# Performance work log

Hardware: AMD Instinct MI355X
Metric: run time of the kernel (lower is better)

Reference implementation:

```python
import jax, jax.numpy as jnp
import numpy as np
import math

D_MODEL = 1024
N_HEAD = 16
D_HEAD = D_MODEL // N_HEAD


def setup_inputs() -> dict:
    key = jax.random.key(0)
    k0, k1, k2, k3, k4 = jax.random.split(key, 5)
    B, N = 4, 2048
    inp = jax.random.normal(k0, (B, N, D_MODEL), dtype=jnp.float32)
    # causal mask: True = keep (masked_fill on ~mask)
    mask = jnp.tril(jnp.ones((N, N), dtype=bool))
    # qkv_proj Linear(d_model, 3*d_model); output Linear(d_model, d_model)
    s_in = 1.0 / math.sqrt(D_MODEL)
    W_qkv = jax.random.uniform(k1, (D_MODEL, 3 * D_MODEL), jnp.float32, -s_in, s_in)
    b_qkv = jax.random.uniform(k2, (3 * D_MODEL,), jnp.float32, -s_in, s_in)
    W_out = jax.random.uniform(k3, (D_MODEL, D_MODEL), jnp.float32, -s_in, s_in)
    b_out = jax.random.uniform(k4, (D_MODEL,), jnp.float32, -s_in, s_in)
    return {"input": inp, "W_qkv": W_qkv, "b_qkv": b_qkv,
            "W_out": W_out, "b_out": b_out, "mask": mask}


def reference(input, W_qkv, b_qkv, W_out, b_out, mask):
    B, N, d = input.shape
    qkv = input @ W_qkv + b_qkv                       # [B,N,3d]  (dropout=eval no-op)
    q, k, v = jnp.split(qkv, 3, axis=-1)
    # [B,N,H,Dh] -> [B,H,N,Dh]
    q = q.reshape(B, N, N_HEAD, D_HEAD).transpose(0, 2, 1, 3)
    k = k.reshape(B, N, N_HEAD, D_HEAD).transpose(0, 2, 1, 3)
    v = v.reshape(B, N, N_HEAD, D_HEAD).transpose(0, 2, 1, 3)
    scale = 1.0 / math.sqrt(D_HEAD)
    scores = jnp.einsum('bhqd,bhkd->bhqk', q, k) * scale   # [B,H,N,N]
    scores = jnp.where(mask, scores, -jnp.inf)
    attn = jax.nn.softmax(scores, axis=-1)
    out = jnp.einsum('bhqk,bhkd->bhqd', attn, v)           # [B,H,N,Dh]
    out = out.transpose(0, 2, 1, 3).reshape(B, N, d)       # concat heads
    return out @ W_out + b_out
```

## Files before the change

### kernel.cpp

```cpp
#include <hip/hip_runtime.h>
#include <hip/hip_bf16.h>

typedef unsigned short u16;
typedef unsigned u32;
typedef __attribute__((ext_vector_type(4))) unsigned short u16x4;
typedef __attribute__((ext_vector_type(8))) unsigned short u16x8;
typedef __attribute__((ext_vector_type(4))) unsigned u32x4;
typedef __attribute__((ext_vector_type(8))) __bf16 bf16x8;
typedef __attribute__((ext_vector_type(4))) float f32x4;

typedef __attribute__((address_space(1))) void as1v;
typedef __attribute__((address_space(3))) void as3v;

#define MFMA16(a, b, c) __builtin_amdgcn_mfma_f32_16x16x32_bf16(a, b, c, 0, 0, 0)

#if __has_builtin(__builtin_amdgcn_permlane16_swap) && __has_builtin(__builtin_amdgcn_permlane32_swap)
#define HAVE_PERMLANE_SWAP 1
#else
#define HAVE_PERMLANE_SWAP 0
#endif

__device__ __forceinline__ u16 f2bf(float f) {
    unsigned u = __builtin_bit_cast(unsigned, f);
    u += 0x7fffu + ((u >> 16) & 1u);
    return (u16)(u >> 16);
}

__device__ __forceinline__ u32 pkbf(float lo, float hi) {
    u32 r;
    asm("v_cvt_pk_bf16_f32 %0, %1, %2" : "=v"(r) : "v"(lo), "v"(hi));
    return r;
}

__device__ __forceinline__ void gload16(const void* g, void* l) {
    __builtin_amdgcn_global_load_lds((as1v*)g, (as3v*)l, 16, 0, 0);
}

__device__ __forceinline__ float redmax_cross(float v) {
#if HAVE_PERMLANE_SWAP
    u32 xu = __builtin_bit_cast(u32, v);
    auto r16 = __builtin_amdgcn_permlane16_swap(xu, xu, false, false);
    float a = fmaxf(__builtin_bit_cast(float, (u32)r16[0]),
                    __builtin_bit_cast(float, (u32)r16[1]));
    u32 au = __builtin_bit_cast(u32, a);
    auto r32 = __builtin_amdgcn_permlane32_swap(au, au, false, false);
    return fmaxf(__builtin_bit_cast(float, (u32)r32[0]),
                 __builtin_bit_cast(float, (u32)r32[1]));
#else
    v = fmaxf(v, __shfl_xor(v, 16, 64));
    return fmaxf(v, __shfl_xor(v, 32, 64));
#endif
}

__device__ __forceinline__ float redsum_cross(float v) {
#if HAVE_PERMLANE_SWAP
    u32 xu = __builtin_bit_cast(u32, v);
    auto r16 = __builtin_amdgcn_permlane16_swap(xu, xu, false, false);
    float a = __builtin_bit_cast(float, (u32)r16[0]) +
              __builtin_bit_cast(float, (u32)r16[1]);
    u32 au = __builtin_bit_cast(u32, a);
    auto r32 = __builtin_amdgcn_permlane32_swap(au, au, false, false);
    return __builtin_bit_cast(float, (u32)r32[0]) +
           __builtin_bit_cast(float, (u32)r32[1]);
#else
    v += __shfl_xor(v, 16, 64);
    return v + __shfl_xor(v, 32, 64);
#endif
}

__global__ void convert_f32_bf16(const float* __restrict__ in, u16* __restrict__ out, int n4) {
    int i = blockIdx.x * blockDim.x + threadIdx.x;
    if (i < n4) {
        float4 v = *(const float4*)&in[(size_t)i * 4];
        u16x4 o;
        o.x = f2bf(v.x); o.y = f2bf(v.y); o.z = f2bf(v.z); o.w = f2bf(v.w);
        *(u16x4*)&out[(size_t)i * 4] = o;
    }
}

__global__ void transpose_convert(const float* __restrict__ in, u16* __restrict__ out, int R, int C) {
    __shared__ float tl[64][65];
    const int rb = blockIdx.x, cb = blockIdx.y;
    const int tid = threadIdx.x;
    for (int it = 0; it < 4; ++it) {
        int lin = (tid + it * 256) * 4;
        int r = lin >> 6, c = lin & 63;
        float4 v = *(const float4*)&in[(size_t)(rb * 64 + r) * C + cb * 64 + c];
        tl[r][c + 0] = v.x; tl[r][c + 1] = v.y; tl[r][c + 2] = v.z; tl[r][c + 3] = v.w;
    }
    __syncthreads();
    for (int it = 0; it < 4; ++it) {
        int lin = (tid + it * 256) * 4;
        int oc = lin >> 6, orr = lin & 63;
        u16x4 o;
        o.x = f2bf(tl[orr + 0][oc]);
        o.y = f2bf(tl[orr + 1][oc]);
        o.z = f2bf(tl[orr + 2][oc]);
        o.w = f2bf(tl[orr + 3][oc]);
        *(u16x4*)&out[(size_t)(cb * 64 + oc) * R + rb * 64 + orr] = o;
    }
}

__global__ void transpose_v(const u16* __restrict__ vbuf, u16* __restrict__ vtb) {
    __shared__ u16 tl[64][65];
    const int nb = blockIdx.x, bh = blockIdx.y;
    const int tid = threadIdx.x;
    for (int it = 0; it < 2; ++it) {
        int lin = (tid + it * 256) * 8;
        int nl = lin >> 6, dh = lin & 63;
        u16x8 v = *(const u16x8*)&vbuf[((size_t)bh * 2048 + nb * 64 + nl) * 64 + dh];
#pragma unroll
        for (int j = 0; j < 8; ++j) tl[dh + j][nl] = v[j];
    }
    __syncthreads();
    for (int it = 0; it < 2; ++it) {
        int lin = (tid + it * 256) * 8;
        int dh = lin >> 6, nl = lin & 63;
        u16x8 o;
#pragma unroll
        for (int j = 0; j < 8; ++j) o[j] = tl[dh][nl + j];
        *(u16x8*)&vtb[((size_t)bh * 64 + dh) * 2048 + nb * 64 + nl] = o;
    }
}

__global__ __launch_bounds__(512, 2) void gemm256_qkv(
    const u16* __restrict__ A, const u16* __restrict__ Bt, const float* __restrict__ bias,
    u16* __restrict__ qb, u16* __restrict__ kb, u16* __restrict__ vb) {
    constexpr int K = 1024;
    constexpr int NT = 32;
    __shared__ u16 ldsu[49152];

    const int bid = blockIdx.x;
    const int swz = (bid & 7) * 96 + (bid >> 3);
    const int bm = swz / 24, bn = swz % 24;

    const int tid = threadIdx.x, wid = tid >> 6, lane = tid & 63;
    const int wr = wid >> 2, wc = wid & 3;
    const int l15 = lane & 15, lhi = lane >> 4;

    const int sslot = (lane & 7) ^ (lane >> 3);
    const int kcol = (sslot & 3) * 8;
    const int mloc = (lane >> 3) * 2 + (sslot >> 2);

    const u16* Arow[2];
#pragma unroll
    for (int li = 0; li < 2; ++li) {
        int sg = wid * 2 + li;
        Arow[li] = A + (size_t)(bm * 256 + sg * 16 + mloc) * K + kcol;
    }
    const u16* Brow = Bt + (size_t)(bn * 128 + wid * 16 + mloc) * K + kcol;

    auto stageA = [&](int buf, int t) {
#pragma unroll
        for (int li = 0; li < 2; ++li) {
            int sg = wid * 2 + li;
            gload16(Arow[li] + t * 32, (char*)ldsu + buf * 24576 + sg * 1024);
        }
    };
    auto stageB = [&](int buf, int t) {
        gload16(Brow + t * 32, (char*)ldsu + buf * 24576 + 16384 + wid * 1024);
    };

    const int rslot = ((l15 & 1) * 4 + lhi) ^ ((l15 >> 1) & 7);
    const int fragoff = (l15 >> 1) * 64 + rslot * 8;

    f32x4 acc[8][2];
#pragma unroll
    for (int i = 0; i < 8; ++i) {
        acc[i][0] = (f32x4){0.f, 0.f, 0.f, 0.f};
        acc[i][1] = (f32x4){0.f, 0.f, 0.f, 0.f};
    }

    auto doTile = [&](int cur, int tstage, bool dostage) {
        const u16* Ab = ldsu + cur * 12288 + wr * 4096 + fragoff;
        const u16* Bb = ldsu + cur * 12288 + 8192 + wc * 1024 + fragoff;
        bf16x8 af[8], b0, b1;
#pragma unroll
        for (int mf = 0; mf < 8; ++mf) af[mf] = *(const bf16x8*)(Ab + mf * 512);
        b0 = *(const bf16x8*)(Bb);
        b1 = *(const bf16x8*)(Bb + 512);
        if (dostage) stageA(tstage & 3, tstage);
        __builtin_amdgcn_s_setprio(1);
#pragma unroll
        for (int mf = 0; mf < 8; ++mf) acc[mf][0] = MFMA16(af[mf], b0, acc[mf][0]);
        __builtin_amdgcn_s_setprio(0);
        if (dostage) stageB(tstage & 3, tstage);
        __builtin_amdgcn_s_setprio(1);
#pragma unroll
        for (int mf = 0; mf < 8; ++mf) acc[mf][1] = MFMA16(af[mf], b1, acc[mf][1]);
        __builtin_amdgcn_s_setprio(0);
    };

    stageA(0, 0); stageB(0, 0);
    stageA(1, 1); stageB(1, 1);
    stageA(2, 2); stageB(2, 2);
    asm volatile("s_waitcnt vmcnt(6)" ::: "memory");
    __builtin_amdgcn_s_barrier();
    __builtin_amdgcn_sched_barrier(0);

    for (int t = 0; t < NT - 3; ++t) {
        doTile(t & 3, t + 3, true);
        asm volatile("s_waitcnt vmcnt(6)" ::: "memory");
        __builtin_amdgcn_s_barrier();
        __builtin_amdgcn_sched_barrier(0);
    }
    doTile((NT - 3) & 3, 0, false);
    asm volatile("s_waitcnt vmcnt(3)" ::: "memory");
    __builtin_amdgcn_s_barrier();
    __builtin_amdgcn_sched_barrier(0);
    doTile((NT - 2) & 3, 0, false);
    asm volatile("s_waitcnt vmcnt(0)" ::: "memory");
    __builtin_amdgcn_s_barrier();
    __builtin_amdgcn_sched_barrier(0);
    doTile((NT - 1) & 3, 0, false);

    __syncthreads();
    const int cg0 = bn * 128 + wc * 32;
    const int which = cg0 >> 10, rem = cg0 & 1023;
    u16* dst = (which == 0) ? qb : (which == 1) ? kb : vb;
    const float qs = (which == 0) ? 0.18033688011112042f : 1.0f;
    const int hh = rem >> 6, dh0 = rem & 63;
    const int rgb0 = bm * 256 + wr * 128;
    const int bb = rgb0 >> 11, n0 = rgb0 & 2047;
    char* lep = (char*)ldsu + wid * 8192;
    float bv0 = bias[cg0 + l15], bv1 = bias[cg0 + 16 + l15];
#pragma unroll
    for (int mf = 0; mf < 8; ++mf)
#pragma unroll
        for (int v = 0; v < 4; ++v) {
            int row = mf * 16 + lhi * 4 + v;
            int sw = ((row >> 2) & 3) << 4;
            *(u16*)(lep + row * 64 + ((l15 * 2) ^ sw)) =
                f2bf((acc[mf][0][v] + bv0) * qs);
            *(u16*)(lep + row * 64 + ((32 + l15 * 2) ^ sw)) =
                f2bf((acc[mf][1][v] + bv1) * qs);
        }
    const size_t gbase = (((size_t)bb * 16 + hh) * 2048 + n0) * 64 + dh0;
#pragma unroll
    for (int it = 0; it < 8; ++it) {
        int idx = it * 64 + lane;
        int row = idx >> 2, j = idx & 3;
        u16x8 vv = *(const u16x8*)(lep + row * 64 + ((j * 16) ^ (((row >> 2) & 3) << 4)));
        *(u16x8*)&dst[gbase + (size_t)row * 64 + j * 8] = vv;
    }
}

__global__ __launch_bounds__(512, 2) void gemm256_out(
    const u16* __restrict__ A, const u16* __restrict__ Bt, const float* __restrict__ bias,
    float* __restrict__ outf) {
    constexpr int K = 1024;
    constexpr int NT = 32;
    __shared__ u16 ldsu[49152];

    const int bid = blockIdx.x;
    const int swz = (bid & 7) * 32 + (bid >> 3);
    const int bm = swz >> 3, bn = swz & 7;

    const int tid = threadIdx.x, wid = tid >> 6, lane = tid & 63;
    const int wr = wid >> 2, wc = wid & 3;
    const int l15 = lane & 15, lhi = lane >> 4;

    const int sslot = (lane & 7) ^ (lane >> 3);
    const int kcol = (sslot & 3) * 8;
    const int mloc = (lane >> 3) * 2 + (sslot >> 2);

    const u16* Arow[2];
#pragma unroll
    for (int li = 0; li < 2; ++li) {
        int sg = wid * 2 + li;
        Arow[li] = A + (size_t)(bm * 256 + sg * 16 + mloc) * K + kcol;
    }
    const u16* Brow = Bt + (size_t)(bn * 128 + wid * 16 + mloc) * K + kcol;

    auto stageA = [&](int buf, int t) {
#pragma unroll
        for (int li = 0; li < 2; ++li) {
            int sg = wid * 2 + li;
            gload16(Arow[li] + t * 32, (char*)ldsu + buf * 24576 + sg * 1024);
        }
    };
    auto stageB = [&](int buf, int t) {
        gload16(Brow + t * 32, (char*)ldsu + buf * 24576 + 16384 + wid * 1024);
    };

    const int rslot = ((l15 & 1) * 4 + lhi) ^ ((l15 >> 1) & 7);
    const int fragoff = (l15 >> 1) * 64 + rslot * 8;

    f32x4 acc[8][2];
#pragma unroll
    for (int i = 0; i < 8; ++i) {
        acc[i][0] = (f32x4){0.f, 0.f, 0.f, 0.f};
        acc[i][1] = (f32x4){0.f, 0.f, 0.f, 0.f};
    }

    auto doTile = [&](int cur, int tstage, bool dostage) {
        const u16* Ab = ldsu + cur * 12288 + wr * 4096 + fragoff;
        const u16* Bb = ldsu + cur * 12288 + 8192 + wc * 1024 + fragoff;
        bf16x8 af[8], b0, b1;
#pragma unroll
        for (int mf = 0; mf < 8; ++mf) af[mf] = *(const bf16x8*)(Ab + mf * 512);
        b0 = *(const bf16x8*)(Bb);
        b1 = *(const bf16x8*)(Bb + 512);
        if (dostage) stageA(tstage & 3, tstage);
        __builtin_amdgcn_s_setprio(1);
#pragma unroll
        for (int mf = 0; mf < 8; ++mf) acc[mf][0] = MFMA16(af[mf], b0, acc[mf][0]);
        __builtin_amdgcn_s_setprio(0);
        if (dostage) stageB(tstage & 3, tstage);
        __builtin_amdgcn_s_setprio(1);
#pragma unroll
        for (int mf = 0; mf < 8; ++mf) acc[mf][1] = MFMA16(af[mf], b1, acc[mf][1]);
        __builtin_amdgcn_s_setprio(0);
    };

    stageA(0, 0); stageB(0, 0);
    stageA(1, 1); stageB(1, 1);
    stageA(2, 2); stageB(2, 2);
    asm volatile("s_waitcnt vmcnt(6)" ::: "memory");
    __builtin_amdgcn_s_barrier();
    __builtin_amdgcn_sched_barrier(0);

    for (int t = 0; t < NT - 3; ++t) {
        doTile(t & 3, t + 3, true);
        asm volatile("s_waitcnt vmcnt(6)" ::: "memory");
        __builtin_amdgcn_s_barrier();
        __builtin_amdgcn_sched_barrier(0);
    }
    doTile((NT - 3) & 3, 0, false);
    asm volatile("s_waitcnt vmcnt(3)" ::: "memory");
    __builtin_amdgcn_s_barrier();
    __builtin_amdgcn_sched_barrier(0);
    doTile((NT - 2) & 3, 0, false);
    asm volatile("s_waitcnt vmcnt(0)" ::: "memory");
    __builtin_amdgcn_s_barrier();
    __builtin_amdgcn_sched_barrier(0);
    doTile((NT - 1) & 3, 0, false);

#pragma unroll
    for (int nf = 0; nf < 2; ++nf) {
        int cg = bn * 128 + wc * 32 + nf * 16 + l15;
        float bv = bias[cg];
#pragma unroll
        for (int mf = 0; mf < 8; ++mf) {
            int rgb = bm * 256 + wr * 128 + mf * 16 + lhi * 4;
#pragma unroll
            for (int v = 0; v < 4; ++v)
                outf[(size_t)(rgb + v) * 1024 + cg] = acc[mf][nf][v] + bv;
        }
    }
}

__global__ __launch_bounds__(256, 4) void attn_kernel(
    const u16* __restrict__ qbuf, const u16* __restrict__ kbuf,
    const u16* __restrict__ vtb, u16* __restrict__ obuf) {
    __shared__ u16 Kl[2][64 * 64];
    __shared__ u16 Vl[2][64 * 64];
    const int bid = blockIdx.x;
    const int rr = bid >> 8;
    const int pp = (bid >> 6) & 3;
    const int c = (rr & 1) ? (((rr >> 1) << 2) + pp)
                           : (15 - ((rr >> 1) << 2) - pp);
    const int bh = ((bid & 7) << 3) + ((bid >> 3) & 7);
    const int b = bh >> 4, h = bh & 15;
    const int tid = threadIdx.x, wid = tid >> 6, lane = tid & 63;
    const int l15 = lane & 15, lhi = lane >> 4;
    const int q0 = c * 128 + wid * 32;
    const int ntW = 2 * c + (wid >> 1) + 1;
    const int ntmax = 2 * c + 2;

    auto loadQ = [&](int qbase, bf16x8* dst) {
        const u16* qp = qbuf + ((size_t)bh * 2048 + qbase + l15) * 64 + lhi * 8;
        dst[0] = *(const bf16x8*)(qp);
        dst[1] = *(const bf16x8*)(qp + 32);
    };
    bf16x8 qf0[2], qf1[2];
    loadQ(q0, qf0); loadQ(q0 + 16, qf1);

    float m0 = -1e30f, l0 = 0.f, m1 = -1e30f, l1 = 0.f;
    f32x4 o0[4], o1[4];
#pragma unroll
    for (int d = 0; d < 4; ++d) {
        o0[d] = (f32x4){0.f, 0.f, 0.f, 0.f};
        o1[d] = (f32x4){0.f, 0.f, 0.f, 0.f};
    }

    const int srow = lane >> 3;
    const int scolb = ((lane & 7) * 16) ^ (srow << 4);

    auto stage = [&](int buf, int t) {
        const int kbase = t * 64;
#pragma unroll
        for (int s = 0; s < 2; ++s) {
            int sg = wid * 2 + s;
            int row = sg * 8 + srow;
            const u16* gk = kbuf + ((size_t)bh * 2048 + kbase + row) * 64 + (scolb >> 1);
            gload16(gk, (char*)Kl[buf] + sg * 1024);
            const u16* gv = vtb + ((size_t)bh * 64 + row) * 2048 + kbase + (scolb >> 1);
            gload16(gv, (char*)Vl[buf] + sg * 1024);
        }
    };

    auto smax = [&](f32x4* s, int qg0, int t, float& m, float& l, f32x4* oa, u32* pw) {
        const int qg = qg0 + l15;
        if (64 * t + 63 > qg0) {
#pragma unroll
            for (int kb4 = 0; kb4 < 4; ++kb4)
#pragma unroll
                for (int v = 0; v < 4; ++v) {
                    int kg = 64 * t + kb4 * 16 + lhi * 4 + v;
                    if (kg > qg) s[kb4][v] = -1e30f;
                }
        }
        float pm = fmaxf(fmaxf(fmaxf(s[0][0], s[0][1]), fmaxf(s[0][2], s[0][3])),
                         fmaxf(fmaxf(s[1][0], s[1][1]), fmaxf(s[1][2], s[1][3])));
        pm = fmaxf(pm, fmaxf(fmaxf(fmaxf(s[2][0], s[2][1]), fmaxf(s[2][2], s[2][3])),
                             fmaxf(fmaxf(s[3][0], s[3][1]), fmaxf(s[3][2], s[3][3]))));
        pm = redmax_cross(pm);
        if (!__all(pm <= m + 8.f)) {
            float nm = fmaxf(m, pm);
            float f = exp2f(m - nm);
            m = nm;
            l *= f;
#pragma unroll
            for (int d = 0; d < 4; ++d)
#pragma unroll
                for (int v = 0; v < 4; ++v) oa[d][v] *= f;
        }
        float rs = 0.f;
#pragma unroll
        for (int kb4 = 0; kb4 < 4; ++kb4)
#pragma unroll
            for (int v = 0; v < 4; ++v) {
                float e = exp2f(s[kb4][v] - m);
                s[kb4][v] = e;
                rs += e;
            }
        l += redsum_cross(rs);
        pw[0] = pkbf(s[0][0], s[0][1]); pw[1] = pkbf(s[0][2], s[0][3]);
        pw[2] = pkbf(s[1][0], s[1][1]); pw[3] = pkbf(s[1][2], s[1][3]);
        pw[4] = pkbf(s[2][0], s[2][1]); pw[5] = pkbf(s[2][2], s[2][3]);
        pw[6] = pkbf(s[3][0], s[3][1]); pw[7] = pkbf(s[3][2], s[3][3]);
    };

    auto computeChunk = [&](const char* Kb, const char* Vb, int t) {
        f32x4 s0[4], s1[4];
        __builtin_amdgcn_s_setprio(1);
#pragma unroll
        for (int kb4 = 0; kb4 < 4; ++kb4) {
            const int r = kb4 * 16 + l15;
            const int sw = (r & 7) << 4;
            const int rowb = r * 128;
            bf16x8 kf0 = *(const bf16x8*)(Kb + rowb + ((lhi * 16) ^ sw));
            bf16x8 kf1 = *(const bf16x8*)(Kb + rowb + ((64 + lhi * 16) ^ sw));
            f32x4 a0 = (f32x4){0.f, 0.f, 0.f, 0.f};
            a0 = MFMA16(kf0, qf0[0], a0);
            a0 = MFMA16(kf1, qf0[1], a0);
            s0[kb4] = a0;
            f32x4 a1 = (f32x4){0.f, 0.f, 0.f, 0.f};
            a1 = MFMA16(kf0, qf1[0], a1);
            a1 = MFMA16(kf1, qf1[1], a1);
            s1[kb4] = a1;
        }
        __builtin_amdgcn_s_setprio(0);
        u32 pw0[8], pw1[8];
        smax(s0, q0, t, m0, l0, o0, pw0);
        smax(s1, q0 + 16, t, m1, l1, o1, pw1);
        __builtin_amdgcn_s_setprio(1);
#pragma unroll
        for (int ks = 0; ks < 2; ++ks) {
            bf16x8 pb0 = __builtin_bit_cast(bf16x8,
                (u32x4){pw0[ks * 4 + 0], pw0[ks * 4 + 1], pw0[ks * 4 + 2], pw0[ks * 4 + 3]});
            bf16x8 pb1 = __builtin_bit_cast(bf16x8,
                (u32x4){pw1[ks * 4 + 0], pw1[ks * 4 + 1], pw1[ks * 4 + 2], pw1[ks * 4 + 3]});
#pragma unroll
            for (int dhb = 0; dhb < 4; ++dhb) {
                const int r = dhb * 16 + l15;
                const int sw = (r & 7) << 4;
                u16x4 v0 = *(const u16x4*)(Vb + r * 128 + ((ks * 64 + 8 * lhi) ^ sw));
                u16x4 v1 = *(const u16x4*)(Vb + r * 128 + ((ks * 64 + 32 + 8 * lhi) ^ sw));
                u16x8 vv = {v0[0], v0[1], v0[2], v0[3], v1[0], v1[1], v1[2], v1[3]};
                bf16x8 vf = __builtin_bit_cast(bf16x8, vv);
                o0[dhb] = MFMA16(vf, pb0, o0[dhb]);
                o1[dhb] = MFMA16(vf, pb1, o1[dhb]);
            }
        }
        __builtin_amdgcn_s_setprio(0);
    };

    stage(0, 0);
    int t = 0;
    for (;;) {
        __syncthreads();
        if (t + 1 < ntmax) stage(1, t + 1);
        if (t < ntW) computeChunk((const char*)Kl[0], (const char*)Vl[0], t);
        if (++t == ntmax) break;
        __syncthreads();
        if (t + 1 < ntmax) stage(0, t + 1);
        if (t < ntW) computeChunk((const char*)Kl[1], (const char*)Vl[1], t);
        if (++t == ntmax) break;
    }

    auto epi = [&](int qg0, float l, const f32x4* oa) {
        const float rl = 1.f / l;
        const int q = qg0 + l15;
        const size_t rowoff = ((size_t)b * 2048 + q) * 1024 + h * 64;
#pragma unroll
        for (int dhb = 0; dhb < 4; ++dhb) {
            u16x4 w;
#pragma unroll
            for (int v = 0; v < 4; ++v) w[v] = f2bf(oa[dhb][v] * rl);
            *(u16x4*)&obuf[rowoff + dhb * 16 + lhi * 4] = w;
        }
    };
    epi(q0, l0, o0);
    epi(q0 + 16, l1, o1);
}

extern "C" void kernel_launch(void* const* d_in, const int* in_sizes, int n_in,
                              void* d_out, int out_size, void* d_ws, size_t ws_size,
                              hipStream_t stream) {
    const float* inp   = (const float*)d_in[0];
    const float* W_qkv = (const float*)d_in[1];
    const float* b_qkv = (const float*)d_in[2];
    const float* W_out = (const float*)d_in[3];
    const float* b_out = (const float*)d_in[4];
    float* out = (float*)d_out;

    u16* xb   = (u16*)d_ws;
    u16* wqt  = xb + 8388608;
    u16* wot  = wqt + 3145728;
    u16* qbuf = wot + 1048576;
    u16* kbuf = qbuf + 8388608;
    u16* vbuf = kbuf + 8388608;
    u16* vtb  = vbuf + 8388608;
    u16* obuf = vtb + 8388608;

    convert_f32_bf16<<<8192, 256, 0, stream>>>(inp, xb, 2097152);
    transpose_convert<<<dim3(16, 48), 256, 0, stream>>>(W_qkv, wqt, 1024, 3072);
    transpose_convert<<<dim3(16, 16), 256, 0, stream>>>(W_out, wot, 1024, 1024);
    gemm256_qkv<<<768, 512, 0, stream>>>(xb, wqt, b_qkv, qbuf, kbuf, vbuf);
    transpose_v<<<dim3(32, 64), 256, 0, stream>>>(vbuf, vtb);
    attn_kernel<<<1024, 256, 0, stream>>>(qbuf, kbuf, vtb, obuf);
    gemm256_out<<<256, 512, 0, stream>>>(obuf, wot, b_out, out);
}
```

Measured before the change: 186.5 us.

## Write V transposed from QKV GEMM epilogue and compute row sums via MFMA

```diff
diff --git a/kernel.cpp b/kernel.cpp
--- a/kernel.cpp
+++ b/kernel.cpp
@@ -101,31 +101,9 @@
     }
 }
 
-__global__ void transpose_v(const u16* __restrict__ vbuf, u16* __restrict__ vtb) {
-    __shared__ u16 tl[64][65];
-    const int nb = blockIdx.x, bh = blockIdx.y;
-    const int tid = threadIdx.x;
-    for (int it = 0; it < 2; ++it) {
-        int lin = (tid + it * 256) * 8;
-        int nl = lin >> 6, dh = lin & 63;
-        u16x8 v = *(const u16x8*)&vbuf[((size_t)bh * 2048 + nb * 64 + nl) * 64 + dh];
-#pragma unroll
-        for (int j = 0; j < 8; ++j) tl[dh + j][nl] = v[j];
-    }
-    __syncthreads();
-    for (int it = 0; it < 2; ++it) {
-        int lin = (tid + it * 256) * 8;
-        int dh = lin >> 6, nl = lin & 63;
-        u16x8 o;
-#pragma unroll
-        for (int j = 0; j < 8; ++j) o[j] = tl[dh][nl + j];
-        *(u16x8*)&vtb[((size_t)bh * 64 + dh) * 2048 + nb * 64 + nl] = o;
-    }
-}
-
 __global__ __launch_bounds__(512, 2) void gemm256_qkv(
     const u16* __restrict__ A, const u16* __restrict__ Bt, const float* __restrict__ bias,
-    u16* __restrict__ qb, u16* __restrict__ kb, u16* __restrict__ vb) {
+    u16* __restrict__ qb, u16* __restrict__ kb, u16* __restrict__ vtb) {
     constexpr int K = 1024;
     constexpr int NT = 32;
     __shared__ u16 ldsu[49152];
@@ -217,31 +195,48 @@
     __syncthreads();
     const int cg0 = bn * 128 + wc * 32;
     const int which = cg0 >> 10, rem = cg0 & 1023;
-    u16* dst = (which == 0) ? qb : (which == 1) ? kb : vb;
-    const float qs = (which == 0) ? 0.18033688011112042f : 1.0f;
     const int hh = rem >> 6, dh0 = rem & 63;
     const int rgb0 = bm * 256 + wr * 128;
     const int bb = rgb0 >> 11, n0 = rgb0 & 2047;
-    char* lep = (char*)ldsu + wid * 8192;
     float bv0 = bias[cg0 + l15], bv1 = bias[cg0 + 16 + l15];
-#pragma unroll
-    for (int mf = 0; mf < 8; ++mf)
-#pragma unroll
-        for (int v = 0; v < 4; ++v) {
-            int row = mf * 16 + lhi * 4 + v;
-            int sw = ((row >> 2) & 3) << 4;
-            *(u16*)(lep + row * 64 + ((l15 * 2) ^ sw)) =
-                f2bf((acc[mf][0][v] + bv0) * qs);
-            *(u16*)(lep + row * 64 + ((32 + l15 * 2) ^ sw)) =
-                f2bf((acc[mf][1][v] + bv1) * qs);
-        }
-    const size_t gbase = (((size_t)bb * 16 + hh) * 2048 + n0) * 64 + dh0;
-#pragma unroll
-    for (int it = 0; it < 8; ++it) {
-        int idx = it * 64 + lane;
-        int row = idx >> 2, j = idx & 3;
-        u16x8 vv = *(const u16x8*)(lep + row * 64 + ((j * 16) ^ (((row >> 2) & 3) << 4)));
-        *(u16x8*)&dst[gbase + (size_t)row * 64 + j * 8] = vv;
+
+    if (which == 2) {
+        const size_t vbase = ((size_t)(bb * 16 + hh) * 64 + dh0) * 2048 + (size_t)n0;
+#pragma unroll
+        for (int nf = 0; nf < 2; ++nf) {
+            float bv = (nf == 0) ? bv0 : bv1;
+            size_t rowb = vbase + (size_t)(nf * 16 + l15) * 2048;
+#pragma unroll
+            for (int mf = 0; mf < 8; ++mf) {
+                u16x4 w;
+#pragma unroll
+                for (int v = 0; v < 4; ++v) w[v] = f2bf(acc[mf][nf][v] + bv);
+                *(u16x4*)&vtb[rowb + mf * 16 + lhi * 4] = w;
+            }
+        }
+    } else {
+        u16* dst = (which == 0) ? qb : kb;
+        const float qs = (which == 0) ? 0.18033688011112042f : 1.0f;
+        char* lep = (char*)ldsu + wid * 8192;
+#pragma unroll
+        for (int mf = 0; mf < 8; ++mf)
+#pragma unroll
+            for (int v = 0; v < 4; ++v) {
+                int row = mf * 16 + lhi * 4 + v;
+                int sw = ((row >> 2) & 3) << 4;
+                *(u16*)(lep + row * 64 + ((l15 * 2) ^ sw)) =
+                    f2bf((acc[mf][0][v] + bv0) * qs);
+                *(u16*)(lep + row * 64 + ((32 + l15 * 2) ^ sw)) =
+                    f2bf((acc[mf][1][v] + bv1) * qs);
+            }
+        const size_t gbase = (((size_t)bb * 16 + hh) * 2048 + n0) * 64 + dh0;
+#pragma unroll
+        for (int it = 0; it < 8; ++it) {
+            int idx = it * 64 + lane;
+            int row = idx >> 2, j = idx & 3;
+            u16x8 vv = *(const u16x8*)(lep + row * 64 + ((j * 16) ^ (((row >> 2) & 3) << 4)));
+            *(u16x8*)&dst[gbase + (size_t)row * 64 + j * 8] = vv;
+        }
     }
 }
 
@@ -376,13 +371,24 @@
     bf16x8 qf0[2], qf1[2];
     loadQ(q0, qf0); loadQ(q0 + 16, qf1);
 
-    float m0 = -1e30f, l0 = 0.f, m1 = -1e30f, l1 = 0.f;
-    f32x4 o0[4], o1[4];
+    bf16x8 onesA;
+    {
+        u16x8 ov;
+        u16 o = (l15 == 0) ? (u16)0x3F80 : (u16)0;
+#pragma unroll
+        for (int j = 0; j < 8; ++j) ov[j] = o;
+        onesA = __builtin_bit_cast(bf16x8, ov);
+    }
+
+    float m0 = -1e30f, m1 = -1e30f;
+    f32x4 o0[4], o1[4], lac0, lac1;
 #pragma unroll
     for (int d = 0; d < 4; ++d) {
         o0[d] = (f32x4){0.f, 0.f, 0.f, 0.f};
         o1[d] = (f32x4){0.f, 0.f, 0.f, 0.f};
     }
+    lac0 = (f32x4){0.f, 0.f, 0.f, 0.f};
+    lac1 = (f32x4){0.f, 0.f, 0.f, 0.f};
 
     const int srow = lane >> 3;
     const int scolb = ((lane & 7) * 16) ^ (srow << 4);
@@ -400,7 +406,7 @@
         }
     };
 
-    auto smax = [&](f32x4* s, int qg0, int t, float& m, float& l, f32x4* oa, u32* pw) {
+    auto smax = [&](f32x4* s, int qg0, int t, float& m, f32x4& lac, f32x4* oa, u32* pw) {
         const int qg = qg0 + l15;
         if (64 * t + 63 > qg0) {
 #pragma unroll
@@ -411,31 +417,29 @@
                     if (kg > qg) s[kb4][v] = -1e30f;
                 }
         }
-        float pm = fmaxf(fmaxf(fmaxf(s[0][0], s[0][1]), fmaxf(s[0][2], s[0][3])),
-                         fmaxf(fmaxf(s[1][0], s[1][1]), fmaxf(s[1][2], s[1][3])));
-        pm = fmaxf(pm, fmaxf(fmaxf(fmaxf(s[2][0], s[2][1]), fmaxf(s[2][2], s[2][3])),
-                             fmaxf(fmaxf(s[3][0], s[3][1]), fmaxf(s[3][2], s[3][3]))));
-        pm = redmax_cross(pm);
+        float f1 = fmaxf(fmaxf(s[0][0], s[0][1]), s[0][2]);
+        float f2 = fmaxf(fmaxf(s[0][3], s[1][0]), s[1][1]);
+        float f3 = fmaxf(fmaxf(s[1][2], s[1][3]), s[2][0]);
+        float f4 = fmaxf(fmaxf(s[2][1], s[2][2]), s[2][3]);
+        float f5 = fmaxf(fmaxf(s[3][0], s[3][1]), s[3][2]);
+        float g1 = fmaxf(fmaxf(f1, f2), f3);
+        float g2 = fmaxf(fmaxf(f4, f5), s[3][3]);
+        float pm = redmax_cross(fmaxf(g1, g2));
         if (!__all(pm <= m + 8.f)) {
             float nm = fmaxf(m, pm);
             float f = exp2f(m - nm);
             m = nm;
-            l *= f;
+#pragma unroll
+            for (int v = 0; v < 4; ++v) lac[v] *= f;
 #pragma unroll
             for (int d = 0; d < 4; ++d)
 #pragma unroll
                 for (int v = 0; v < 4; ++v) oa[d][v] *= f;
         }
-        float rs = 0.f;
 #pragma unroll
         for (int kb4 = 0; kb4 < 4; ++kb4)
 #pragma unroll
-            for (int v = 0; v < 4; ++v) {
-                float e = exp2f(s[kb4][v] - m);
-                s[kb4][v] = e;
-                rs += e;
-            }
-        l += redsum_cross(rs);
+            for (int v = 0; v < 4; ++v) s[kb4][v] = exp2f(s[kb4][v] - m);
         pw[0] = pkbf(s[0][0], s[0][1]); pw[1] = pkbf(s[0][2], s[0][3]);
         pw[2] = pkbf(s[1][0], s[1][1]); pw[3] = pkbf(s[1][2], s[1][3]);
         pw[4] = pkbf(s[2][0], s[2][1]); pw[5] = pkbf(s[2][2], s[2][3]);
@@ -463,8 +467,8 @@
         }
         __builtin_amdgcn_s_setprio(0);
         u32 pw0[8], pw1[8];
-        smax(s0, q0, t, m0, l0, o0, pw0);
-        smax(s1, q0 + 16, t, m1, l1, o1, pw1);
+        smax(s0, q0, t, m0, lac0, o0, pw0);
+        smax(s1, q0 + 16, t, m1, lac1, o1, pw1);
         __builtin_amdgcn_s_setprio(1);
 #pragma unroll
         for (int ks = 0; ks < 2; ++ks) {
@@ -483,6 +487,8 @@
                 o0[dhb] = MFMA16(vf, pb0, o0[dhb]);
                 o1[dhb] = MFMA16(vf, pb1, o1[dhb]);
             }
+            lac0 = MFMA16(onesA, pb0, lac0);
+            lac1 = MFMA16(onesA, pb1, lac1);
         }
         __builtin_amdgcn_s_setprio(0);
     };
@@ -500,7 +506,8 @@
         if (++t == ntmax) break;
     }
 
-    auto epi = [&](int qg0, float l, const f32x4* oa) {
+    auto epi = [&](int qg0, const f32x4& lac, const f32x4* oa) {
+        float l = redsum_cross(lac[0] + lac[1] + lac[2] + lac[3]);
         const float rl = 1.f / l;
         const int q = qg0 + l15;
         const size_t rowoff = ((size_t)b * 2048 + q) * 1024 + h * 64;
@@ -512,8 +519,8 @@
             *(u16x4*)&obuf[rowoff + dhb * 16 + lhi * 4] = w;
         }
     };
-    epi(q0, l0, o0);
-    epi(q0 + 16, l1, o1);
+    epi(q0, lac0, o0);
+    epi(q0 + 16, lac1, o1);
 }
 
 extern "C" void kernel_launch(void* const* d_in, const int* in_sizes, int n_in,
@@ -531,15 +538,13 @@
     u16* wot  = wqt + 3145728;
     u16* qbuf = wot + 1048576;
     u16* kbuf = qbuf + 8388608;
-    u16* vbuf = kbuf + 8388608;
-    u16* vtb  = vbuf + 8388608;
+    u16* vtb  = kbuf + 8388608;
     u16* obuf = vtb + 8388608;
 
     convert_f32_bf16<<<8192, 256, 0, stream>>>(inp, xb, 2097152);
     transpose_convert<<<dim3(16, 48), 256, 0, stream>>>(W_qkv, wqt, 1024, 3072);
     transpose_convert<<<dim3(16, 16), 256, 0, stream>>>(W_out, wot, 1024, 1024);
-    gemm256_qkv<<<768, 512, 0, stream>>>(xb, wqt, b_qkv, qbuf, kbuf, vbuf);
-    transpose_v<<<dim3(32, 64), 256, 0, stream>>>(vbuf, vtb);
+    gemm256_qkv<<<768, 512, 0, stream>>>(xb, wqt, b_qkv, qbuf, kbuf, vtb);
     attn_kernel<<<1024, 256, 0, stream>>>(qbuf, kbuf, vtb, obuf);
     gemm256_out<<<256, 512, 0, stream>>>(obuf, wot, b_out, out);
 }
```

Result: no change. 186.5 us (-0.0%).
